# Performance work log

Measured on AMD Instinct MI355X. Metric: run time of the kernel, lower is better.

## Reference

```python
import jax, jax.numpy as jnp
import numpy as np

NEG_INF = -1e30  # stands in for float('-inf'); avoids nan in masked softmax edge cases


def setup_inputs() -> dict:
    key = jax.random.key(0)
    ks = jax.random.split(key, 6)
    B, N, MD, QD, AD = 64, 512, 1024, 1024, 1024
    stdv_m = 1.0 / np.sqrt(MD)
    stdv_q = 1.0 / np.sqrt(QD)
    stdv_a = 1.0 / np.sqrt(AD)
    return {
        "memory_values": jax.random.normal(ks[0], (B, N, MD), dtype=jnp.float32),
        "mask": jax.random.randint(ks[1], (B, N), 0, 2, dtype=jnp.int32),
        "query": jax.random.normal(ks[2], (B, QD), dtype=jnp.float32),
        "Wh": jax.random.uniform(ks[3], (MD, AD), jnp.float32, -stdv_m, stdv_m),
        "Ws": jax.random.uniform(ks[4], (QD, AD), jnp.float32, -stdv_q, stdv_q),
        "v": jax.random.uniform(ks[5], (AD, 1), jnp.float32, -stdv_a, stdv_a),
    }


def reference(memory_values, mask, query, Wh, Ws, v):
    # Et(i) = tanh(Hi*Wh + St*Ws) @ v ; At = softmax(Et) with masking
    tq = query @ Ws                                   # (B, AD)
    h = jnp.tanh(memory_values @ Wh + tq[:, None, :])  # (B, N, AD)
    logits = jnp.squeeze(h @ v, axis=-1)              # (B, N)

    maskf = mask.astype(logits.dtype)
    # no_cells[b] == 1 iff every cell in row b is masked out
    no_cells = jnp.prod(1.0 - maskf, axis=1, keepdims=True)  # (B, 1)
    suppress = jnp.where(maskf == 0, NEG_INF, 0.0)
    suppress = jnp.where(no_cells == 1.0, 0.0, suppress)
    weights = jax.nn.softmax(logits + suppress, axis=-1)
    weights = jnp.where(no_cells == 1.0, 0.0, weights)

    context = jnp.einsum("bn,bnd->bd", weights, memory_values)
    return context
```

## Files before the change

kernel.cpp:

```cpp
#include <hip/hip_runtime.h>
#include <cstdint>
#include <cstddef>

typedef float floatx4 __attribute__((ext_vector_type(4)));
typedef _Float16 half8_t __attribute__((ext_vector_type(8)));
typedef _Float16 half2_t __attribute__((ext_vector_type(2)));

#define AS1 __attribute__((address_space(1)))
#define AS3 __attribute__((address_space(3)))

__device__ __forceinline__ void glds16(const void* g, void* l) {
  __builtin_amdgcn_global_load_lds((const AS1 void*)g, (AS3 void*)l, 16, 0, 0);
}

__device__ __forceinline__ half2_t pkrtz(float a, float b) {
  return __builtin_bit_cast(half2_t, __builtin_amdgcn_cvt_pkrtz(a, b));
}

__device__ __forceinline__ float fast_tanh(float x) {
  float e2 = __expf(2.f * x);
  return 1.f - 2.f * __builtin_amdgcn_rcpf(e2 + 1.f);
}

__global__ void kp_cvt(const float* __restrict__ mem, _Float16* __restrict__ memh) {
  size_t i = ((size_t)(blockIdx.x << 8) + threadIdx.x) << 3;
  floatx4 a = *(const floatx4*)(mem + i);
  floatx4 b = *(const floatx4*)(mem + i + 4);
  union { half2_t h2[4]; half8_t h8; } u;
  u.h2[0] = half2_t{(_Float16)a[0], (_Float16)a[1]};
  u.h2[1] = half2_t{(_Float16)a[2], (_Float16)a[3]};
  u.h2[2] = half2_t{(_Float16)b[0], (_Float16)b[1]};
  u.h2[3] = half2_t{(_Float16)b[2], (_Float16)b[3]};
  *(half8_t*)(memh + i) = u.h8;
}

__global__ void k0_transpose(const float* __restrict__ Wh, _Float16* __restrict__ WhT) {
  __shared__ float t[64][65];
  int k0 = blockIdx.y << 6, n0 = blockIdx.x << 6;
  int tx = threadIdx.x, ty = threadIdx.y;
  #pragma unroll
  for (int r = ty; r < 64; r += 4) t[r][tx] = Wh[(size_t)(k0 + r) * 1024 + n0 + tx];
  __syncthreads();
  #pragma unroll
  for (int r = ty; r < 64; r += 4)
    WhT[(size_t)(n0 + r) * 1024 + k0 + tx] = (_Float16)t[tx][r];
}

__global__ __launch_bounds__(256) void k1_tq(const float* __restrict__ q,
                                             const float* __restrict__ Ws,
                                             float* __restrict__ tq) {
  __shared__ float qs[1024];
  __shared__ float red[4][64];
  int b = blockIdx.y;
  int d0 = blockIdx.x << 6;
  int dl = threadIdx.x & 63, kg = threadIdx.x >> 6;
  for (int k = threadIdx.x; k < 1024; k += 256) qs[k] = q[(b << 10) + k];
  __syncthreads();
  float acc = 0.f;
  int kbase = kg << 8;
  #pragma unroll 8
  for (int k = 0; k < 256; ++k)
    acc += qs[kbase + k] * Ws[(size_t)(kbase + k) * 1024 + d0 + dl];
  red[kg][dl] = acc;
  __syncthreads();
  if (kg == 0)
    tq[(b << 10) + d0 + dl] = red[0][dl] + red[1][dl] + red[2][dl] + red[3][dl];
}

__global__ __launch_bounds__(256, 2) void k2_gemm_h(
    const _Float16* __restrict__ Ah, const _Float16* __restrict__ BT,
    const float* __restrict__ tq, const float* __restrict__ v,
    float* __restrict__ partials) {
  __shared__ _Float16 As[128 * 32];
  __shared__ _Float16 Bs[128 * 32];
  const int bid = blockIdx.x;
  const int mtile = ((bid >> 6) << 3) | (bid & 7);
  const int nblk = (bid >> 3) & 7;
  const int m0 = mtile << 7, n0 = nblk << 7;
  const int tid = threadIdx.x;
  const int w = tid >> 6, lane = tid & 63;
  const int wm = w >> 1, wn = w & 1, quad = lane >> 4, l15 = lane & 15;

  floatx4 acc[4][4];
  #pragma unroll
  for (int i = 0; i < 4; ++i)
    #pragma unroll
    for (int j = 0; j < 4; ++j) acc[i][j] = floatx4{0.f, 0.f, 0.f, 0.f};

  const _Float16 *gA[2], *gB[2];
  _Float16 *lA[2], *lB[2];
  #pragma unroll
  for (int t = 0; t < 2; ++t) {
    int L = (t << 8) + (w << 6) + lane;
    int row = L >> 2, jj = L & 3;
    int j = (jj - row - (row >> 2)) & 3;
    gA[t] = Ah + (size_t)(m0 + row) * 1024 + (j << 3);
    gB[t] = BT + (size_t)(n0 + row) * 1024 + (j << 3);
    lA[t] = As + (t << 11) + (w << 9);
    lB[t] = Bs + (t << 11) + (w << 9);
  }

  const half8_t *aaddr[4], *baddr[4];
  #pragma unroll
  for (int i = 0; i < 4; ++i) {
    int ar = (wm << 6) + (i << 4) + l15;
    aaddr[i] = (const half8_t*)(As + (ar << 5) + (((quad + ar + (ar >> 2)) & 3) << 3));
    int br = (wn << 6) + (i << 4) + l15;
    baddr[i] = (const half8_t*)(Bs + (br << 5) + (((quad + br + (br >> 2)) & 3) << 3));
  }

  for (int k0 = 0; k0 < 1024; k0 += 32) {
    __syncthreads();
    glds16(gA[0] + k0, lA[0]);
    glds16(gA[1] + k0, lA[1]);
    glds16(gB[0] + k0, lB[0]);
    glds16(gB[1] + k0, lB[1]);
    __syncthreads();
    half8_t af[4], bfr[4];
    #pragma unroll
    for (int i = 0; i < 4; ++i) af[i] = *aaddr[i];
    #pragma unroll
    for (int j = 0; j < 4; ++j) bfr[j] = *baddr[j];
    #pragma unroll
    for (int i = 0; i < 4; ++i)
      #pragma unroll
      for (int j = 0; j < 4; ++j)
        acc[i][j] = __builtin_amdgcn_mfma_f32_16x16x32_f16(af[i], bfr[j], acc[i][j], 0, 0, 0);
  }

  const int b = m0 >> 9;
  const int colbase = n0 + (wn << 6) + l15;
  float tqv[4], vv[4];
  #pragma unroll
  for (int j = 0; j < 4; ++j) {
    int n = colbase + (j << 4);
    tqv[j] = tq[(b << 10) + n];
    vv[j] = v[n];
  }
  #pragma unroll
  for (int i = 0; i < 4; ++i) {
    #pragma unroll
    for (int r = 0; r < 4; ++r) {
      float s = 0.f;
      #pragma unroll
      for (int j = 0; j < 4; ++j) s += fast_tanh(acc[i][j][r] + tqv[j]) * vv[j];
      s += __shfl_xor(s, 1);
      s += __shfl_xor(s, 2);
      s += __shfl_xor(s, 4);
      s += __shfl_xor(s, 8);
      if (l15 == 0) {
        int m = m0 + (wm << 6) + (i << 4) + (quad << 2) + r;
        partials[m * 16 + (nblk << 1) + wn] = s;
      }
    }
  }
}

__global__ __launch_bounds__(256, 2) void k2_gemm_f32(
    const float* __restrict__ A, const _Float16* __restrict__ BT,
    const float* __restrict__ tq, const float* __restrict__ v,
    float* __restrict__ partials) {
  __shared__ float As[128 * 32];
  __shared__ _Float16 Bs[128 * 32];
  const int bid = blockIdx.x;
  const int mtile = ((bid >> 6) << 3) | (bid & 7);
  const int nblk = (bid >> 3) & 7;
  const int m0 = mtile << 7, n0 = nblk << 7;
  const int tid = threadIdx.x;
  const int w = tid >> 6, lane = tid & 63;
  const int wm = w >> 1, wn = w & 1, quad = lane >> 4, l15 = lane & 15;

  floatx4 acc[4][4];
  #pragma unroll
  for (int i = 0; i < 4; ++i)
    #pragma unroll
    for (int j = 0; j < 4; ++j) acc[i][j] = floatx4{0.f, 0.f, 0.f, 0.f};

  const float* gA[4];
  float* lA[4];
  #pragma unroll
  for (int t = 0; t < 4; ++t) {
    int L = (t << 8) + (w << 6) + lane;
    int row = L >> 3, jj = L & 7;
    int j = (jj - row) & 7;
    gA[t] = A + (size_t)(m0 + row) * 1024 + (j << 2);
    lA[t] = As + (t << 10) + (w << 8);
  }
  const _Float16* gB[2];
  _Float16* lB[2];
  #pragma unroll
  for (int t = 0; t < 2; ++t) {
    int L = (t << 8) + (w << 6) + lane;
    int row = L >> 2, jj = L & 3;
    int j = (jj - row - (row >> 2)) & 3;
    gB[t] = BT + (size_t)(n0 + row) * 1024 + (j << 3);
    lB[t] = Bs + (t << 11) + (w << 9);
  }
  const floatx4* aaddr[4][2];
  #pragma unroll
  for (int i = 0; i < 4; ++i) {
    int row = (wm << 6) + (i << 4) + l15;
    #pragma unroll
    for (int h = 0; h < 2; ++h) {
      int pos = ((quad << 1) + h + row) & 7;
      aaddr[i][h] = (const floatx4*)(As + (row << 5) + (pos << 2));
    }
  }
  const half8_t* baddr[4];
  #pragma unroll
  for (int j = 0; j < 4; ++j) {
    int row = (wn << 6) + (j << 4) + l15;
    int pos = (quad + row + (row >> 2)) & 3;
    baddr[j] = (const half8_t*)(Bs + (row << 5) + (pos << 3));
  }
  for (int k0 = 0; k0 < 1024; k0 += 32) {
    __syncthreads();
    glds16(gA[0] + k0, lA[0]);
    glds16(gA[1] + k0, lA[1]);
    glds16(gA[2] + k0, lA[2]);
    glds16(gA[3] + k0, lA[3]);
    glds16(gB[0] + k0, lB[0]);
    glds16(gB[1] + k0, lB[1]);
    __syncthreads();
    half8_t af[4], bfr[4];
    #pragma unroll
    for (int i = 0; i < 4; ++i) {
      floatx4 x = *aaddr[i][0], y = *aaddr[i][1];
      union { half2_t h2[4]; half8_t h8; } u;
      u.h2[0] = pkrtz(x[0], x[1]);
      u.h2[1] = pkrtz(x[2], x[3]);
      u.h2[2] = pkrtz(y[0], y[1]);
      u.h2[3] = pkrtz(y[2], y[3]);
      af[i] = u.h8;
    }
    #pragma unroll
    for (int j = 0; j < 4; ++j) bfr[j] = *baddr[j];
    #pragma unroll
    for (int i = 0; i < 4; ++i)
      #pragma unroll
      for (int j = 0; j < 4; ++j)
        acc[i][j] = __builtin_amdgcn_mfma_f32_16x16x32_f16(af[i], bfr[j], acc[i][j], 0, 0, 0);
  }
  const int b = m0 >> 9;
  const int colbase = n0 + (wn << 6) + l15;
  float tqv[4], vv[4];
  #pragma unroll
  for (int j = 0; j < 4; ++j) {
    int n = colbase + (j << 4);
    tqv[j] = tq[(b << 10) + n];
    vv[j] = v[n];
  }
  #pragma unroll
  for (int i = 0; i < 4; ++i) {
    #pragma unroll
    for (int r = 0; r < 4; ++r) {
      float s = 0.f;
      #pragma unroll
      for (int j = 0; j < 4; ++j) s += fast_tanh(acc[i][j][r] + tqv[j]) * vv[j];
      s += __shfl_xor(s, 1);
      s += __shfl_xor(s, 2);
      s += __shfl_xor(s, 4);
      s += __shfl_xor(s, 8);
      if (l15 == 0) {
        int m = m0 + (wm << 6) + (i << 4) + (quad << 2) + r;
        partials[m * 16 + (nblk << 1) + wn] = s;
      }
    }
  }
}

__global__ __launch_bounds__(512) void k3_softmax(const float* __restrict__ partials,
                                                  const int* __restrict__ mask,
                                                  float* __restrict__ weights) {
  int b = blockIdx.x;
  int n = threadIdx.x;
  int m = (b << 9) + n;
  float s = 0.f;
  #pragma unroll
  for (int i = 0; i < 16; ++i) s += partials[m * 16 + i];
  int mk = mask[m];
  float logit = mk ? s : -1e30f;
  __shared__ float red[8];
  float x = logit;
  #pragma unroll
  for (int off = 32; off > 0; off >>= 1) x = fmaxf(x, __shfl_xor(x, off));
  if ((n & 63) == 0) red[n >> 6] = x;
  __syncthreads();
  float mx = red[0];
  #pragma unroll
  for (int i = 1; i < 8; ++i) mx = fmaxf(mx, red[i]);
  float e = mk ? __expf(logit - mx) : 0.f;
  float ss = e;
  #pragma unroll
  for (int off = 32; off > 0; off >>= 1) ss += __shfl_xor(ss, off);
  __syncthreads();
  if ((n & 63) == 0) red[n >> 6] = ss;
  __syncthreads();
  float tot = 0.f;
  #pragma unroll
  for (int i = 0; i < 8; ++i) tot += red[i];
  weights[m] = (tot > 0.f) ? e / tot : 0.f;
}

__global__ void k4_ctx_h(const _Float16* __restrict__ memh,
                         const float* __restrict__ weights, float* __restrict__ ctxp) {
  int nc = blockIdx.x, b = blockIdx.y;
  int d = threadIdx.x << 3;
  float acc[8] = {0.f, 0.f, 0.f, 0.f, 0.f, 0.f, 0.f, 0.f};
  int nbase = nc << 5;
  for (int n = nbase; n < nbase + 32; ++n) {
    float wv = weights[(b << 9) + n];
    half8_t x = *(const half8_t*)(memh + ((size_t)((b << 9) + n) << 10) + d);
    #pragma unroll
    for (int k = 0; k < 8; ++k) acc[k] += wv * (float)x[k];
  }
  float* o = ctxp + ((size_t)((b << 4) + nc) << 10) + d;
  #pragma unroll
  for (int k = 0; k < 8; ++k) o[k] = acc[k];
}

__global__ void k5_reduce16(const float* __restrict__ ctxp, float* __restrict__ out) {
  int i = (blockIdx.x << 8) + threadIdx.x;
  int b = i >> 10, d = i & 1023;
  float s = 0.f;
  #pragma unroll
  for (int cc = 0; cc < 16; ++cc) s += ctxp[((size_t)((b << 4) + cc) << 10) + d];
  out[i] = s;
}

__global__ void k4_ctx_f32(const float* __restrict__ mem, const float* __restrict__ weights,
                           float* __restrict__ ctxp) {
  int nc = blockIdx.x, b = blockIdx.y;
  int d = threadIdx.x << 3;
  floatx4 a0 = {0.f, 0.f, 0.f, 0.f}, a1 = {0.f, 0.f, 0.f, 0.f};
  int nbase = nc << 6;
  for (int n = nbase; n < nbase + 64; ++n) {
    float wv = weights[(b << 9) + n];
    const floatx4* p = (const floatx4*)(mem + ((size_t)((b << 9) + n) << 10) + d);
    a0 += wv * p[0];
    a1 += wv * p[1];
  }
  floatx4* o = (floatx4*)(ctxp + ((size_t)((b << 3) + nc) << 10) + d);
  o[0] = a0;
  o[1] = a1;
}

__global__ void k5_reduce8(const float* __restrict__ ctxp, float* __restrict__ out) {
  int i = (blockIdx.x << 8) + threadIdx.x;
  int b = i >> 10, d = i & 1023;
  float s = 0.f;
  #pragma unroll
  for (int cc = 0; cc < 8; ++cc) s += ctxp[((size_t)((b << 3) + cc) << 10) + d];
  out[i] = s;
}

extern "C" void kernel_launch(void* const* d_in, const int* in_sizes, int n_in,
                              void* d_out, int out_size, void* d_ws, size_t ws_size,
                              hipStream_t stream) {
  const float* mem = (const float*)d_in[0];
  const int* mask = (const int*)d_in[1];
  const float* query = (const float*)d_in[2];
  const float* Wh = (const float*)d_in[3];
  const float* Ws = (const float*)d_in[4];
  const float* v = (const float*)d_in[5];
  float* out = (float*)d_out;

  char* ws = (char*)d_ws;
  const size_t need16 = (73ull << 20);

  if (ws_size >= need16) {
    _Float16* memh = (_Float16*)ws;
    _Float16* WhT = (_Float16*)(ws + (64ull << 20));
    float* partials = (float*)(ws + (66ull << 20));
    float* tq = (float*)(ws + (68ull << 20));
    float* weights = (float*)(ws + (68ull << 20) + (256 << 10));
    float* ctxp = (float*)(ws + (69ull << 20));

    kp_cvt<<<16384, 256, 0, stream>>>(mem, memh);
    k0_transpose<<<dim3(16, 16), dim3(64, 4), 0, stream>>>(Wh, WhT);
    k1_tq<<<dim3(16, 64), 256, 0, stream>>>(query, Ws, tq);
    k2_gemm_h<<<2048, 256, 0, stream>>>(memh, WhT, tq, v, partials);
    k3_softmax<<<64, 512, 0, stream>>>(partials, mask, weights);
    k4_ctx_h<<<dim3(16, 64), 128, 0, stream>>>(memh, weights, ctxp);
    k5_reduce16<<<256, 256, 0, stream>>>(ctxp, out);
  } else {
    _Float16* WhT = (_Float16*)ws;
    float* partials = (float*)(ws + ((size_t)2 << 20));
    float* tq = (float*)(ws + ((size_t)4 << 20));
    float* weights = (float*)(ws + ((size_t)4 << 20) + (256 << 10));
    float* ctxp = (float*)(ws + ((size_t)9 << 19));

    k0_transpose<<<dim3(16, 16), dim3(64, 4), 0, stream>>>(Wh, WhT);
    k1_tq<<<dim3(16, 64), 256, 0, stream>>>(query, Ws, tq);
    k2_gemm_f32<<<2048, 256, 0, stream>>>(mem, WhT, tq, v, partials);
    k3_softmax<<<64, 512, 0, stream>>>(partials, mask, weights);
    k4_ctx_f32<<<dim3(8, 64), 128, 0, stream>>>(mem, weights, ctxp);
    k5_reduce8<<<256, 256, 0, stream>>>(ctxp, out);
  }
}
```

Before: 339.9 us.

## Add 256x256 eight-wave pipelined MFMA GEMM and fuse prep kernels into one launch

Replaces the 128x128 fp16 GEMM with a 256x256-tile kernel using 512 threads and 128KB of dynamic LDS. It double-buffers global-to-LDS loads across four phases per k-group, interleaved with MFMA work and explicit vmcnt waits. It also merges the fp32-to-fp16 conversion, the Wh transpose and the query projection into a single launch with block-index dispatch. The aims are more data reuse per tile, better overlap of loads with math, and fewer launches, at the cost of high register and LDS pressure and tricky manual synchronisation.

Measured after the change: 306.5 us. -9.8%, faster.

```diff
diff --git a/kernel.cpp b/kernel.cpp
--- a/kernel.cpp
+++ b/kernel.cpp
@@ -22,16 +22,52 @@
   return 1.f - 2.f * __builtin_amdgcn_rcpf(e2 + 1.f);
 }
 
-__global__ void kp_cvt(const float* __restrict__ mem, _Float16* __restrict__ memh) {
-  size_t i = ((size_t)(blockIdx.x << 8) + threadIdx.x) << 3;
-  floatx4 a = *(const floatx4*)(mem + i);
-  floatx4 b = *(const floatx4*)(mem + i + 4);
-  union { half2_t h2[4]; half8_t h8; } u;
-  u.h2[0] = half2_t{(_Float16)a[0], (_Float16)a[1]};
-  u.h2[1] = half2_t{(_Float16)a[2], (_Float16)a[3]};
-  u.h2[2] = half2_t{(_Float16)b[0], (_Float16)b[1]};
-  u.h2[3] = half2_t{(_Float16)b[2], (_Float16)b[3]};
-  *(half8_t*)(memh + i) = u.h8;
+__global__ __launch_bounds__(256) void k_prep(
+    const float* __restrict__ mem, _Float16* __restrict__ memh,
+    const float* __restrict__ Wh, _Float16* __restrict__ WhT,
+    const float* __restrict__ q, const float* __restrict__ Ws,
+    float* __restrict__ tq) {
+  __shared__ float sh[64 * 65];
+  const int bx = blockIdx.x;
+  const int tid = threadIdx.x;
+  if (bx < 16384) {
+    size_t i = (((size_t)bx << 8) + tid) << 3;
+    floatx4 a = *(const floatx4*)(mem + i);
+    floatx4 b = *(const floatx4*)(mem + i + 4);
+    union { half2_t h2[4]; half8_t h8; } u;
+    u.h2[0] = half2_t{(_Float16)a[0], (_Float16)a[1]};
+    u.h2[1] = half2_t{(_Float16)a[2], (_Float16)a[3]};
+    u.h2[2] = half2_t{(_Float16)b[0], (_Float16)b[1]};
+    u.h2[3] = half2_t{(_Float16)b[2], (_Float16)b[3]};
+    *(half8_t*)(memh + i) = u.h8;
+  } else if (bx < 16640) {
+    int bb = bx - 16384;
+    int n0 = (bb & 15) << 6, k0 = (bb >> 4) << 6;
+    int tx = tid & 63, ty = tid >> 6;
+    #pragma unroll
+    for (int r = ty; r < 64; r += 4) sh[r * 65 + tx] = Wh[(size_t)(k0 + r) * 1024 + n0 + tx];
+    __syncthreads();
+    #pragma unroll
+    for (int r = ty; r < 64; r += 4)
+      WhT[(size_t)(n0 + r) * 1024 + k0 + tx] = (_Float16)sh[tx * 65 + r];
+  } else {
+    int bb = bx - 16640;
+    int d0 = (bb & 15) << 6, b = bb >> 4;
+    int dl = tid & 63, kg = tid >> 6;
+    float* qs = sh;
+    float* red = sh + 1024;
+    for (int k = tid; k < 1024; k += 256) qs[k] = q[(b << 10) + k];
+    __syncthreads();
+    float acc = 0.f;
+    int kbase = kg << 8;
+    #pragma unroll 8
+    for (int k = 0; k < 256; ++k)
+      acc += qs[kbase + k] * Ws[(size_t)(kbase + k) * 1024 + d0 + dl];
+    red[(kg << 6) + dl] = acc;
+    __syncthreads();
+    if (kg == 0)
+      tq[(b << 10) + d0 + dl] = red[dl] + red[64 + dl] + red[128 + dl] + red[192 + dl];
+  }
 }
 
 __global__ void k0_transpose(const float* __restrict__ Wh, _Float16* __restrict__ WhT) {
@@ -67,6 +103,170 @@
     tq[(b << 10) + d0 + dl] = red[0][dl] + red[1][dl] + red[2][dl] + red[3][dl];
 }
 
+__global__ __launch_bounds__(512, 2) void k2_8ph(
+    const _Float16* __restrict__ Ah, const _Float16* __restrict__ BT,
+    const float* __restrict__ tq, const float* __restrict__ v,
+    float* __restrict__ partials) {
+  extern __shared__ char smem[];
+  const int bid = blockIdx.x;
+  const int wg = ((bid & 7) << 6) | (bid >> 3);
+  const int mtile = wg >> 2, ntile = wg & 3;
+  const int m0 = mtile << 8, n0 = ntile << 8;
+  const int tid = threadIdx.x;
+  const int w = tid >> 6, lane = tid & 63;
+  const int wm = w >> 2, wn = w & 3, quad = lane >> 4, l15 = lane & 15;
+
+  int aoff[2][4], boff[2][2];
+  #pragma unroll
+  for (int ks = 0; ks < 2; ++ks) {
+    int swz = ((ks << 2) + quad) ^ (l15 & 7);
+    #pragma unroll
+    for (int i = 0; i < 4; ++i)
+      aoff[ks][i] = (wm << 14) + (((i << 4) + l15) << 7) + (swz << 4);
+    #pragma unroll
+    for (int j = 0; j < 2; ++j)
+      boff[ks][j] = 65536 + (wn << 12) + (((j << 4) + l15) << 7) + (swz << 4);
+  }
+
+  const int rr = tid >> 3, cc = tid & 7;
+  const int r5 = rr & 31;
+  int aSrc[2][2], bSrc[2][2], dA[2][2], dB[2][2];
+  #pragma unroll
+  for (int h = 0; h < 2; ++h)
+    #pragma unroll
+    for (int hm = 0; hm < 2; ++hm) {
+      aSrc[h][hm] = ((m0 + (hm << 7) + (h << 6) + rr) << 10) + ((cc ^ (rr & 7)) << 3);
+      dA[h][hm] = (((hm << 1) + h) << 13) + (w << 10);
+    }
+  #pragma unroll
+  for (int ch = 0; ch < 2; ++ch)
+    #pragma unroll
+    for (int is = 0; is < 2; ++is) {
+      int wnb = (is << 1) + (rr >> 5);
+      bSrc[ch][is] = ((n0 + (wnb << 6) + (ch << 5) + r5) << 10) + ((cc ^ (r5 & 7)) << 3);
+      dB[ch][is] = 65536 + (ch << 14) + (is << 13) + (w << 10);
+    }
+
+  floatx4 acc[8][4];
+  #pragma unroll
+  for (int i = 0; i < 8; ++i)
+    #pragma unroll
+    for (int j = 0; j < 4; ++j) acc[i][j] = floatx4{0.f, 0.f, 0.f, 0.f};
+
+  half8_t af[2][4], bf[2][2][2];
+
+#define STAGE_A(H, KST, OO)                                   \
+  glds16(Ah + aSrc[H][0] + (KST), smem + (OO) + dA[H][0]);    \
+  glds16(Ah + aSrc[H][1] + (KST), smem + (OO) + dA[H][1]);
+#define STAGE_B(CH, KST, OO)                                  \
+  glds16(BT + bSrc[CH][0] + (KST), smem + (OO) + dB[CH][0]);  \
+  glds16(BT + bSrc[CH][1] + (KST), smem + (OO) + dB[CH][1]);
+#define VMCNT4 asm volatile("s_waitcnt vmcnt(4)" ::: "memory");
+#define LOAD_AF(CO, RHOFF)                                    \
+  _Pragma("unroll")                                           \
+  for (int ks_ = 0; ks_ < 2; ++ks_) {                         \
+    _Pragma("unroll")                                         \
+    for (int i_ = 0; i_ < 4; ++i_)                            \
+      af[ks_][i_] = *(const half8_t*)(smem + (CO) + (RHOFF) + aoff[ks_][i_]); \
+  }
+#define LOAD_BF(CH, CO, CHOFF)                                \
+  _Pragma("unroll")                                           \
+  for (int ks_ = 0; ks_ < 2; ++ks_) {                         \
+    _Pragma("unroll")                                         \
+    for (int j_ = 0; j_ < 2; ++j_)                            \
+      bf[CH][ks_][j_] = *(const half8_t*)(smem + (CO) + (CHOFF) + boff[ks_][j_]); \
+  }
+#define PHASE(RH, CH)                                         \
+  __builtin_amdgcn_s_barrier();                               \
+  asm volatile("s_waitcnt lgkmcnt(0)" ::: "memory");          \
+  __builtin_amdgcn_s_setprio(1);                              \
+  _Pragma("unroll")                                           \
+  for (int i_ = 0; i_ < 4; ++i_) {                            \
+    _Pragma("unroll")                                         \
+    for (int j_ = 0; j_ < 2; ++j_)                            \
+      acc[(RH)*4 + i_][(CH)*2 + j_] = __builtin_amdgcn_mfma_f32_16x16x32_f16( \
+          af[0][i_], bf[CH][0][j_], acc[(RH)*4 + i_][(CH)*2 + j_], 0, 0, 0);  \
+  }                                                           \
+  _Pragma("unroll")                                           \
+  for (int i_ = 0; i_ < 4; ++i_) {                            \
+    _Pragma("unroll")                                         \
+    for (int j_ = 0; j_ < 2; ++j_)                            \
+      acc[(RH)*4 + i_][(CH)*2 + j_] = __builtin_amdgcn_mfma_f32_16x16x32_f16( \
+          af[1][i_], bf[CH][1][j_], acc[(RH)*4 + i_][(CH)*2 + j_], 0, 0, 0);  \
+  }                                                           \
+  __builtin_amdgcn_s_setprio(0);                              \
+  __builtin_amdgcn_s_barrier();
+#define GROUP(CO, OO, KST)  \
+  LOAD_AF(CO, 0)            \
+  LOAD_BF(0, CO, 0)         \
+  STAGE_A(0, KST, OO)       \
+  VMCNT4                    \
+  PHASE(0, 0)               \
+  LOAD_BF(1, CO, 16384)     \
+  STAGE_B(0, KST, OO)       \
+  VMCNT4                    \
+  PHASE(0, 1)               \
+  LOAD_AF(CO, 8192)         \
+  STAGE_B(1, KST, OO)       \
+  PHASE(1, 0)               \
+  STAGE_A(1, KST, OO)       \
+  VMCNT4                    \
+  PHASE(1, 1)
+
+  STAGE_A(0, 0, 0)
+  STAGE_B(0, 0, 0)
+  STAGE_B(1, 0, 0)
+  STAGE_A(1, 0, 0)
+  VMCNT4
+  __builtin_amdgcn_s_barrier();
+
+  #pragma unroll 1
+  for (int g2 = 0; g2 < 8; ++g2) {
+    const int g = g2 << 1;
+    const int kst1 = (g + 1) << 6;
+    const int kst2 = (g2 == 7) ? (15 << 6) : ((g + 2) << 6);
+    GROUP(0, 32768, kst1)
+    GROUP(32768, 0, kst2)
+  }
+
+#undef GROUP
+#undef PHASE
+#undef LOAD_BF
+#undef LOAD_AF
+#undef VMCNT4
+#undef STAGE_B
+#undef STAGE_A
+
+  asm volatile("s_waitcnt vmcnt(0)" ::: "memory");
+
+  const int b = m0 >> 9;
+  const int colb = n0 + (wn << 6) + l15;
+  float tqv[4], vv[4];
+  #pragma unroll
+  for (int jf = 0; jf < 4; ++jf) {
+    int n = colb + (jf << 4);
+    tqv[jf] = tq[(b << 10) + n];
+    vv[jf] = v[n];
+  }
+  #pragma unroll
+  for (int rf = 0; rf < 8; ++rf) {
+    #pragma unroll
+    for (int r = 0; r < 4; ++r) {
+      float s = 0.f;
+      #pragma unroll
+      for (int jf = 0; jf < 4; ++jf) s += fast_tanh(acc[rf][jf][r] + tqv[jf]) * vv[jf];
+      s += __shfl_xor(s, 1);
+      s += __shfl_xor(s, 2);
+      s += __shfl_xor(s, 4);
+      s += __shfl_xor(s, 8);
+      if (l15 == 0) {
+        int m = m0 + (wm << 7) + (rf << 4) + (quad << 2) + r;
+        partials[m * 16 + (ntile << 2) + wn] = s;
+      }
+    }
+  }
+}
+
 __global__ __launch_bounds__(256, 2) void k2_gemm_h(
     const _Float16* __restrict__ Ah, const _Float16* __restrict__ BT,
     const float* __restrict__ tq, const float* __restrict__ v,
@@ -376,10 +576,18 @@
     float* weights = (float*)(ws + (68ull << 20) + (256 << 10));
     float* ctxp = (float*)(ws + (69ull << 20));
 
-    kp_cvt<<<16384, 256, 0, stream>>>(mem, memh);
-    k0_transpose<<<dim3(16, 16), dim3(64, 4), 0, stream>>>(Wh, WhT);
-    k1_tq<<<dim3(16, 64), 256, 0, stream>>>(query, Ws, tq);
-    k2_gemm_h<<<2048, 256, 0, stream>>>(memh, WhT, tq, v, partials);
+    static int use8 = -1;
+    if (use8 < 0) {
+      use8 = (hipFuncSetAttribute((const void*)k2_8ph,
+                                  hipFuncAttributeMaxDynamicSharedMemorySize,
+                                  131072) == hipSuccess) ? 1 : 0;
+    }
+
+    k_prep<<<17664, 256, 0, stream>>>(mem, memh, Wh, WhT, query, Ws, tq);
+    if (use8)
+      k2_8ph<<<512, 512, 131072, stream>>>(memh, WhT, tq, v, partials);
+    else
+      k2_gemm_h<<<2048, 256, 0, stream>>>(memh, WhT, tq, v, partials);
     k3_softmax<<<64, 512, 0, stream>>>(partials, mask, weights);
     k4_ctx_h<<<dim3(16, 64), 128, 0, stream>>>(memh, weights, ctxp);
     k5_reduce16<<<256, 256, 0, stream>>>(ctxp, out);
```
